# Performance work log

Measured on AMD Instinct MI355X. Metric: run time of the kernel, lower is better.

Reference implementation:

```python
import jax, jax.numpy as jnp
import numpy as np

TEMPERATURE = 8.0  # sqrt(head_dim=64)
NEG_FILL = -1000000000.0

def setup_inputs() -> dict:
    key = jax.random.key(0)
    k1, k2, k3, k4, k5 = jax.random.split(key, 5)
    B, H, S, D = 4, 16, 1024, 64
    q = jax.random.normal(k1, (B, H, S, D), dtype=jnp.float32)
    k = jax.random.normal(k2, (B, H, S, D), dtype=jnp.float32)
    v = jax.random.normal(k3, (B, H, S, D), dtype=jnp.float32)
    similarity = jax.random.normal(k4, (B, H, S, S), dtype=jnp.float32)
    mask = jax.random.randint(k5, (B, 1, S, S), 0, 2).astype(bool)
    return {"q": q, "k": k, "v": v, "similarity": similarity, "mask": mask}

def reference(q, k, v, similarity, mask):
    # scores: [B,H,S,S] = (q/temp) @ k^T
    attn = jnp.einsum('bhqd,bhkd->bhqk', q / TEMPERATURE, k)
    attn = jnp.where(mask, NEG_FILL, attn)          # masked_fill (mask broadcasts over heads)
    attn = jax.nn.softmax(attn + similarity, axis=-1)  # dropout p=0 (eval): identity
    output = jnp.einsum('bhqk,bhkd->bhqd', attn, v)
    return (output, attn)
```

## Files before the change

### kernel.cpp

```cpp
#include <hip/hip_runtime.h>
#include <stdint.h>


#define S_LEN 1024
#define D_DIM 64
#define QT 16
#define NEG_FILL (-1000000000.0f)
#define LOG2E 1.44269504088896340736f
#define SIMSTR 4160

typedef __bf16 bf16x8 __attribute__((ext_vector_type(8)));
typedef float f32x4 __attribute__((ext_vector_type(4)));
typedef unsigned short u16x4 __attribute__((ext_vector_type(4)));

__device__ __forceinline__ unsigned short f2bf(float x) {
    unsigned u = __builtin_bit_cast(unsigned, x);
    u += 0x7fffu + ((u >> 16) & 1u);
    return (unsigned short)(u >> 16);
}
__device__ __forceinline__ float bf2f(unsigned short b) {
    return __builtin_bit_cast(float, (unsigned)b << 16);
}

__device__ __forceinline__ void dma16(const void* g, void* l) {
    __builtin_amdgcn_global_load_lds(
        (const __attribute__((address_space(1))) unsigned int*)g,
        (__attribute__((address_space(3))) unsigned int*)l, 16, 0, 0);
}

__device__ __forceinline__ unsigned short* sptr(unsigned short* s, int row, int col) {
    return (unsigned short*)((char*)s + row * 2048 + ((col * 2) ^ ((row & 7) << 4)));
}

__global__ void prep_qkm(const float* __restrict__ q, const float* __restrict__ k,
                         const void* __restrict__ mraw,
                         unsigned short* __restrict__ Qb, unsigned short* __restrict__ Kb,
                         unsigned char* __restrict__ Mb)
{
    const int t = threadIdx.x;
    const int i = blockIdx.x * 256 + t;
    f32x4 q4 = ((const f32x4*)q)[i];
    f32x4 k4 = ((const f32x4*)k)[i];
    u16x4 qo, ko;
#pragma unroll
    for (int j = 0; j < 4; ++j) {
        qo[j] = f2bf(q4[j] * 0.125f);
        ko[j] = f2bf(k4[j]);
    }
    ((u16x4*)Qb)[i] = qo;
    ((u16x4*)Kb)[i] = ko;

    __shared__ int s_not_int, s_not_f32;
    if (t == 0) { s_not_int = 0; s_not_f32 = 0; }
    __syncthreads();
    const unsigned* wdd = (const unsigned*)mraw;
    int ni = 0, nf = 0;
    for (int j = t; j < 1024; j += 256) {
        unsigned x = wdd[j];
        if (x > 1u) ni = 1;
        if (x != 0u && x != 0x3f800000u) nf = 1;
    }
    if (ni) s_not_int = 1;
    if (nf) s_not_f32 = 1;
    __syncthreads();
    const int fmt = (s_not_int == 0) ? 0 : ((s_not_f32 == 0) ? 1 : 2);
    uchar4 o;
    if (fmt == 0) {
        int4 x = ((const int4*)mraw)[i];
        o.x = x.x ? 1 : 0; o.y = x.y ? 1 : 0; o.z = x.z ? 1 : 0; o.w = x.w ? 1 : 0;
    } else if (fmt == 1) {
        float4 x = ((const float4*)mraw)[i];
        o.x = (x.x != 0.f) ? 1 : 0; o.y = (x.y != 0.f) ? 1 : 0;
        o.z = (x.z != 0.f) ? 1 : 0; o.w = (x.w != 0.f) ? 1 : 0;
    } else {
        uchar4 x = ((const uchar4*)mraw)[i];
        o.x = x.x ? 1 : 0; o.y = x.y ? 1 : 0; o.z = x.z ? 1 : 0; o.w = x.w ? 1 : 0;
    }
    ((uchar4*)Mb)[i] = o;
}

__global__ void prep_vt(const float* __restrict__ v, unsigned short* __restrict__ Vt)
{
    __shared__ unsigned short sT[64 * 72];
    const int bh = blockIdx.x >> 4;
    const int st = blockIdx.x & 15;
    const int t = threadIdx.x;
    const float* vb = v + (size_t)(bh * S_LEN + st * 64) * D_DIM;
#pragma unroll
    for (int p = 0; p < 4; ++p) {
        int lin = p * 256 + t;
        int r = lin >> 4;
        int c = lin & 15;
        f32x4 x = ((const f32x4*)(vb + r * D_DIM))[c];
        unsigned short* dst = &sT[r * 72 + c * 4];
#pragma unroll
        for (int j = 0; j < 4; ++j) dst[j] = f2bf(x[j]);
    }
    __syncthreads();
    unsigned short* ob = Vt + (size_t)bh * D_DIM * S_LEN + st * 64;
#pragma unroll
    for (int p = 0; p < 4; ++p) {
        int lin = p * 256 + t;
        int d = lin >> 4;
        int s4 = (lin & 15) * 4;
        u16x4 o;
#pragma unroll
        for (int j = 0; j < 4; ++j) o[j] = sT[(s4 + j) * 72 + d];
        *(u16x4*)&ob[d * S_LEN + s4] = o;
    }
}

__global__ __launch_bounds__(256, 2)
void attn_main(const float* __restrict__ simg_, const unsigned short* __restrict__ Qb,
               const unsigned short* __restrict__ Kb, const unsigned short* __restrict__ Vtb,
               const unsigned char* __restrict__ Mb, float* __restrict__ out,
               float* __restrict__ attn)
{
    __shared__ __align__(16) unsigned char smem[16 * SIMSTR + 512];

    const int blk = ((blockIdx.x & 7) << 9) | (blockIdx.x >> 3);
    const int bh = blk >> 6;
    const int qt = blk & 63;
    const int b = bh >> 4;
    const int t = threadIdx.x;
    const int w = t >> 6;
    const int lane = t & 63;
    const int quad = lane >> 4;
    const int l15 = lane & 15;
    const int n0 = w * 16;

    const unsigned short* Qg = Qb + (size_t)(bh * S_LEN + qt * QT) * D_DIM;
    const unsigned short* Kg = Kb + (size_t)bh * S_LEN * D_DIM;
    const unsigned short* Vg = Vtb + (size_t)bh * D_DIM * S_LEN;
    const float* simg = simg_ + ((size_t)(bh * S_LEN + qt * QT)) * S_LEN;
    const unsigned char* mg = Mb + ((size_t)(b * S_LEN + qt * QT)) * S_LEN;
    float* attng = attn + ((size_t)(bh * S_LEN + qt * QT)) * S_LEN;

#pragma unroll
    for (int rr = 0; rr < 4; ++rr) {
        const float* gr = simg + (size_t)(w * 4 + rr) * S_LEN + lane * 4;
        unsigned char* lr = smem + (w * 4 + rr) * SIMSTR;
#pragma unroll
        for (int c = 0; c < 4; ++c)
            dma16(gr + c * 256, lr + c * 1024);
    }

    const bf16x8 av0 = *(const bf16x8*)&Qg[l15 * D_DIM + quad * 8];
    const bf16x8 av1 = *(const bf16x8*)&Qg[l15 * D_DIM + 32 + quad * 8];
    f32x4 acc[16];
#pragma unroll
    for (int kt = 0; kt < 16; ++kt) {
        const unsigned short* kp = &Kg[(size_t)(kt * 64 + n0 + l15) * D_DIM + quad * 8];
        bf16x8 kv0 = *(const bf16x8*)kp;
        bf16x8 kv1 = *(const bf16x8*)(kp + 32);
        f32x4 a = {0.f, 0.f, 0.f, 0.f};
        a = __builtin_amdgcn_mfma_f32_16x16x32_bf16(av0, kv0, a, 0, 0, 0);
        a = __builtin_amdgcn_mfma_f32_16x16x32_bf16(av1, kv1, a, 0, 0, 0);
        acc[kt] = a;
    }

    unsigned char mk[16][4];
#pragma unroll
    for (int kt = 0; kt < 16; ++kt)
#pragma unroll
        for (int r = 0; r < 4; ++r)
            mk[kt][r] = mg[(size_t)(quad * 4 + r) * S_LEN + kt * 64 + n0 + l15];

    __syncthreads();

#pragma unroll
    for (int kt = 0; kt < 16; ++kt)
#pragma unroll
        for (int r = 0; r < 4; ++r) {
            float sv = *(const float*)(smem + (quad * 4 + r) * SIMSTR
                                       + (size_t)(kt * 64 + n0 + l15) * 4);
            acc[kt][r] = mk[kt][r] ? NEG_FILL : (acc[kt][r] + sv);
        }

    float* cmbMax = (float*)(smem + 16 * SIMSTR);
    float* cmbSum = (float*)(smem + 16 * SIMSTR + 256);
    float pm[4];
#pragma unroll
    for (int r = 0; r < 4; ++r) {
        float m = acc[0][r];
#pragma unroll
        for (int kt = 1; kt < 16; ++kt) m = fmaxf(m, acc[kt][r]);
#pragma unroll
        for (int off = 1; off <= 8; off <<= 1)
            m = fmaxf(m, __shfl_xor(m, off, 64));
        pm[r] = m;
    }
    if (l15 == 0) {
        f32x4 v = {pm[0], pm[1], pm[2], pm[3]};
        *(f32x4*)&cmbMax[w * 16 + quad * 4] = v;
    }
    __syncthreads();
    float rM[4];
#pragma unroll
    for (int r = 0; r < 4; ++r) {
        const int row = quad * 4 + r;
        rM[r] = fmaxf(fmaxf(cmbMax[row], cmbMax[16 + row]),
                      fmaxf(cmbMax[32 + row], cmbMax[48 + row]));
    }

    float ps[4] = {0.f, 0.f, 0.f, 0.f};
#pragma unroll
    for (int kt = 0; kt < 16; ++kt)
#pragma unroll
        for (int r = 0; r < 4; ++r) {
            float e = __builtin_amdgcn_exp2f((acc[kt][r] - rM[r]) * LOG2E);
            acc[kt][r] = e;
            ps[r] += e;
        }
#pragma unroll
    for (int r = 0; r < 4; ++r)
#pragma unroll
        for (int off = 1; off <= 8; off <<= 1)
            ps[r] += __shfl_xor(ps[r], off, 64);
    if (l15 == 0) {
        f32x4 v = {ps[0], ps[1], ps[2], ps[3]};
        *(f32x4*)&cmbSum[w * 16 + quad * 4] = v;
    }
    __syncthreads();
    float rinv[4];
#pragma unroll
    for (int r = 0; r < 4; ++r) {
        const int row = quad * 4 + r;
        rinv[r] = 1.0f / ((cmbSum[row] + cmbSum[16 + row]) +
                          (cmbSum[32 + row] + cmbSum[48 + row]));
    }

    unsigned short* pL = (unsigned short*)smem;
#pragma unroll
    for (int kt = 0; kt < 16; ++kt)
#pragma unroll
        for (int r = 0; r < 4; ++r) {
            float p = acc[kt][r] * rinv[r];
            acc[kt][r] = p;
            *sptr(pL, quad * 4 + r, kt * 64 + n0 + l15) = f2bf(p);
        }
    __syncthreads();

    const int d0 = w * 16;
    f32x4 oa0 = {0.f, 0.f, 0.f, 0.f}, oa1 = {0.f, 0.f, 0.f, 0.f};
#pragma unroll
    for (int kt = 0; kt < 16; kt += 2) {
        const unsigned short* vp0 = &Vg[(size_t)(d0 + l15) * S_LEN + kt * 64 + quad * 8];
        bf16x8 x0 = *(const bf16x8*)vp0;
        bf16x8 x1 = *(const bf16x8*)(vp0 + 32);
        bf16x8 y0 = *(const bf16x8*)(vp0 + 64);
        bf16x8 y1 = *(const bf16x8*)(vp0 + 96);
        bf16x8 pa0 = *(const bf16x8*)sptr(pL, l15, kt * 64 + quad * 8);
        bf16x8 pa1 = *(const bf16x8*)sptr(pL, l15, kt * 64 + 32 + quad * 8);
        bf16x8 pb0 = *(const bf16x8*)sptr(pL, l15, kt * 64 + 64 + quad * 8);
        bf16x8 pb1 = *(const bf16x8*)sptr(pL, l15, kt * 64 + 96 + quad * 8);
        oa0 = __builtin_amdgcn_mfma_f32_16x16x32_bf16(pa0, x0, oa0, 0, 0, 0);
        oa0 = __builtin_amdgcn_mfma_f32_16x16x32_bf16(pa1, x1, oa0, 0, 0, 0);
        oa1 = __builtin_amdgcn_mfma_f32_16x16x32_bf16(pb0, y0, oa1, 0, 0, 0);
        oa1 = __builtin_amdgcn_mfma_f32_16x16x32_bf16(pb1, y1, oa1, 0, 0, 0);
    }
    f32x4 oacc = oa0 + oa1;

    float* og = out + ((size_t)(bh * S_LEN + qt * QT)) * D_DIM;
#pragma unroll
    for (int r = 0; r < 4; ++r)
        __builtin_nontemporal_store(oacc[r], &og[(quad * 4 + r) * D_DIM + d0 + l15]);

#pragma unroll
    for (int kt = 0; kt < 16; ++kt)
#pragma unroll
        for (int r = 0; r < 4; ++r)
            __builtin_nontemporal_store(acc[kt][r],
                &attng[(size_t)(quad * 4 + r) * S_LEN + kt * 64 + n0 + l15]);
}

extern "C" void kernel_launch(void* const* d_in, const int* in_sizes, int n_in,
                              void* d_out, int out_size, void* d_ws, size_t ws_size,
                              hipStream_t stream)
{
    const float* q = (const float*)d_in[0];
    const float* k = (const float*)d_in[1];
    const float* v = (const float*)d_in[2];
    const float* sim = (const float*)d_in[3];
    const void* mask = d_in[4];
    float* out = (float*)d_out;
    float* attn = out + (size_t)4 * 16 * 1024 * 64;

    char* ws = (char*)d_ws;
    unsigned short* Qb = (unsigned short*)(ws + (size_t)0);
    unsigned short* Kb = (unsigned short*)(ws + ((size_t)8 << 20));
    unsigned short* Vt = (unsigned short*)(ws + ((size_t)16 << 20));
    unsigned char*  Mb = (unsigned char*)(ws + ((size_t)24 << 20));

    prep_qkm<<<4096, 256, 0, stream>>>(q, k, mask, Qb, Kb, Mb);
    prep_vt<<<1024, 256, 0, stream>>>(v, Vt);
    attn_main<<<4096, 256, 0, stream>>>(sim, Qb, Kb, Vt, Mb, out, attn);
}
```

Before: 620.5 us.

## Load similarity directly from global, shrink LDS, and vectorize attn stores

```diff
diff --git a/kernel.cpp b/kernel.cpp
--- a/kernel.cpp
+++ b/kernel.cpp
@@ -7,7 +7,6 @@
 #define QT 16
 #define NEG_FILL (-1000000000.0f)
 #define LOG2E 1.44269504088896340736f
-#define SIMSTR 4160
 
 typedef __bf16 bf16x8 __attribute__((ext_vector_type(8)));
 typedef float f32x4 __attribute__((ext_vector_type(4)));
@@ -22,11 +21,19 @@
     return __builtin_bit_cast(float, (unsigned)b << 16);
 }
 
-__device__ __forceinline__ void dma16(const void* g, void* l) {
-    __builtin_amdgcn_global_load_lds(
-        (const __attribute__((address_space(1))) unsigned int*)g,
-        (__attribute__((address_space(3))) unsigned int*)l, 16, 0, 0);
-}
+__device__ __forceinline__ float gloadf_nt(const void* p) {
+    float d;
+    asm volatile("global_load_dword %0, %1, off nt" : "=v"(d) : "v"(p) : "memory");
+    return d;
+}
+__device__ __forceinline__ unsigned gloadub(const void* p) {
+    unsigned d;
+    asm volatile("global_load_ubyte %0, %1, off" : "=v"(d) : "v"(p) : "memory");
+    return d;
+}
+#define WAITV0 do { \
+    asm volatile("s_waitcnt vmcnt(0)" ::: "memory"); \
+    __builtin_amdgcn_sched_barrier(0); } while (0)
 
 __device__ __forceinline__ unsigned short* sptr(unsigned short* s, int row, int col) {
     return (unsigned short*)((char*)s + row * 2048 + ((col * 2) ^ ((row & 7) << 4)));
@@ -110,13 +117,14 @@
     }
 }
 
-__global__ __launch_bounds__(256, 2)
+__global__ __launch_bounds__(256, 4)
 void attn_main(const float* __restrict__ simg_, const unsigned short* __restrict__ Qb,
                const unsigned short* __restrict__ Kb, const unsigned short* __restrict__ Vtb,
                const unsigned char* __restrict__ Mb, float* __restrict__ out,
                float* __restrict__ attn)
 {
-    __shared__ __align__(16) unsigned char smem[16 * SIMSTR + 512];
+    __shared__ __align__(16) unsigned short sS[QT * S_LEN];
+    __shared__ __align__(16) float cmb[128];
 
     const int blk = ((blockIdx.x & 7) << 9) | (blockIdx.x >> 3);
     const int bh = blk >> 6;
@@ -136,15 +144,6 @@
     const unsigned char* mg = Mb + ((size_t)(b * S_LEN + qt * QT)) * S_LEN;
     float* attng = attn + ((size_t)(bh * S_LEN + qt * QT)) * S_LEN;
 
-#pragma unroll
-    for (int rr = 0; rr < 4; ++rr) {
-        const float* gr = simg + (size_t)(w * 4 + rr) * S_LEN + lane * 4;
-        unsigned char* lr = smem + (w * 4 + rr) * SIMSTR;
-#pragma unroll
-        for (int c = 0; c < 4; ++c)
-            dma16(gr + c * 256, lr + c * 1024);
-    }
-
     const bf16x8 av0 = *(const bf16x8*)&Qg[l15 * D_DIM + quad * 8];
     const bf16x8 av1 = *(const bf16x8*)&Qg[l15 * D_DIM + 32 + quad * 8];
     f32x4 acc[16];
@@ -159,26 +158,28 @@
         acc[kt] = a;
     }
 
-    unsigned char mk[16][4];
-#pragma unroll
-    for (int kt = 0; kt < 16; ++kt)
-#pragma unroll
-        for (int r = 0; r < 4; ++r)
-            mk[kt][r] = mg[(size_t)(quad * 4 + r) * S_LEN + kt * 64 + n0 + l15];
-
-    __syncthreads();
-
-#pragma unroll
-    for (int kt = 0; kt < 16; ++kt)
-#pragma unroll
-        for (int r = 0; r < 4; ++r) {
-            float sv = *(const float*)(smem + (quad * 4 + r) * SIMSTR
-                                       + (size_t)(kt * 64 + n0 + l15) * 4);
-            acc[kt][r] = mk[kt][r] ? NEG_FILL : (acc[kt][r] + sv);
-        }
-
-    float* cmbMax = (float*)(smem + 16 * SIMSTR);
-    float* cmbSum = (float*)(smem + 16 * SIMSTR + 256);
+#pragma unroll
+    for (int C = 0; C < 16; C += 4) {
+        float sv_[4][4];
+        unsigned mk_[4][4];
+#pragma unroll
+        for (int kk = 0; kk < 4; ++kk)
+#pragma unroll
+            for (int r = 0; r < 4; ++r) {
+                const size_t off = (size_t)(quad * 4 + r) * S_LEN + (C + kk) * 64 + n0 + l15;
+                sv_[kk][r] = gloadf_nt(simg + off);
+                mk_[kk][r] = gloadub(mg + off);
+            }
+        WAITV0;
+#pragma unroll
+        for (int kk = 0; kk < 4; ++kk)
+#pragma unroll
+            for (int r = 0; r < 4; ++r)
+                acc[C + kk][r] = mk_[kk][r] ? NEG_FILL : (acc[C + kk][r] + sv_[kk][r]);
+    }
+
+    float* cmbMax = cmb;
+    float* cmbSum = cmb + 64;
     float pm[4];
 #pragma unroll
     for (int r = 0; r < 4; ++r) {
@@ -230,15 +231,11 @@
                           (cmbSum[32 + row] + cmbSum[48 + row]));
     }
 
-    unsigned short* pL = (unsigned short*)smem;
 #pragma unroll
     for (int kt = 0; kt < 16; ++kt)
 #pragma unroll
-        for (int r = 0; r < 4; ++r) {
-            float p = acc[kt][r] * rinv[r];
-            acc[kt][r] = p;
-            *sptr(pL, quad * 4 + r, kt * 64 + n0 + l15) = f2bf(p);
-        }
+        for (int r = 0; r < 4; ++r)
+            *sptr(sS, quad * 4 + r, kt * 64 + n0 + l15) = f2bf(acc[kt][r] * rinv[r]);
     __syncthreads();
 
     const int d0 = w * 16;
@@ -250,10 +247,10 @@
         bf16x8 x1 = *(const bf16x8*)(vp0 + 32);
         bf16x8 y0 = *(const bf16x8*)(vp0 + 64);
         bf16x8 y1 = *(const bf16x8*)(vp0 + 96);
-        bf16x8 pa0 = *(const bf16x8*)sptr(pL, l15, kt * 64 + quad * 8);
-        bf16x8 pa1 = *(const bf16x8*)sptr(pL, l15, kt * 64 + 32 + quad * 8);
-        bf16x8 pb0 = *(const bf16x8*)sptr(pL, l15, kt * 64 + 64 + quad * 8);
-        bf16x8 pb1 = *(const bf16x8*)sptr(pL, l15, kt * 64 + 96 + quad * 8);
+        bf16x8 pa0 = *(const bf16x8*)sptr(sS, l15, kt * 64 + quad * 8);
+        bf16x8 pa1 = *(const bf16x8*)sptr(sS, l15, kt * 64 + 32 + quad * 8);
+        bf16x8 pb0 = *(const bf16x8*)sptr(sS, l15, kt * 64 + 64 + quad * 8);
+        bf16x8 pb1 = *(const bf16x8*)sptr(sS, l15, kt * 64 + 96 + quad * 8);
         oa0 = __builtin_amdgcn_mfma_f32_16x16x32_bf16(pa0, x0, oa0, 0, 0, 0);
         oa0 = __builtin_amdgcn_mfma_f32_16x16x32_bf16(pa1, x1, oa0, 0, 0, 0);
         oa1 = __builtin_amdgcn_mfma_f32_16x16x32_bf16(pb0, y0, oa1, 0, 0, 0);
@@ -267,11 +264,16 @@
         __builtin_nontemporal_store(oacc[r], &og[(quad * 4 + r) * D_DIM + d0 + l15]);
 
 #pragma unroll
-    for (int kt = 0; kt < 16; ++kt)
-#pragma unroll
-        for (int r = 0; r < 4; ++r)
-            __builtin_nontemporal_store(acc[kt][r],
-                &attng[(size_t)(quad * 4 + r) * S_LEN + kt * 64 + n0 + l15]);
+    for (int rr = 0; rr < 4; ++rr) {
+        const int row = w * 4 + rr;
+#pragma unroll
+        for (int j = 0; j < 4; ++j) {
+            const int col = j * 256 + lane * 4;
+            u16x4 x = *(const u16x4*)sptr(sS, row, col);
+            f32x4 p = { bf2f(x[0]), bf2f(x[1]), bf2f(x[2]), bf2f(x[3]) };
+            __builtin_nontemporal_store(p, (f32x4*)&attng[(size_t)row * S_LEN + col]);
+        }
+    }
 }
 
 extern "C" void kernel_launch(void* const* d_in, const int* in_sizes, int n_in,
```

Result: no change. 617.0 us (-0.6%).
